# Kernel tuning notes

Hardware: AMD Instinct MI355X
Metric: run time of the kernel (lower is better)

Reference implementation:

```python
import jax, jax.numpy as jnp
import numpy as np
import math

D_MODEL = 512
N_HEADS = 8
D_FF = 2048
EPS = 1e-5

def _layernorm(x, g, b):
    m = jnp.mean(x, axis=-1, keepdims=True)
    v = jnp.var(x, axis=-1, keepdims=True)
    return (x - m) * jax.lax.rsqrt(v + EPS) * g + b

def setup_inputs() -> dict:
    key = jax.random.key(0)
    ks = jax.random.split(key, 8)
    d, dff = D_MODEL, D_FF
    s = lambda fan: 1.0 / math.sqrt(fan)
    return {
        "x": jax.random.normal(ks[0], (4, 2048, d), dtype=jnp.float32),
        "w_qkv": jax.random.normal(ks[1], (d, 3 * d), dtype=jnp.float32) * s(d),
        "b_qkv": jnp.zeros((3 * d,), dtype=jnp.float32),
        "w1": jax.random.normal(ks[2], (d, dff), dtype=jnp.float32) * s(d),
        "b1": jnp.zeros((dff,), dtype=jnp.float32),
        "w2": jax.random.normal(ks[3], (dff, d), dtype=jnp.float32) * s(dff),
        "b2": jnp.zeros((d,), dtype=jnp.float32),
        "g1": jnp.ones((d,), dtype=jnp.float32),
        "be1": jnp.zeros((d,), dtype=jnp.float32),
        "g2": jnp.ones((d,), dtype=jnp.float32),
        "be2": jnp.zeros((d,), dtype=jnp.float32),
    }

def reference(x, w_qkv, b_qkv, w1, b1, w2, b2, g1, be1, g2, be2):
    B, L, d = x.shape
    H = N_HEADS
    hd = d // H
    # Faithful to original: scale = 1/sqrt(hd), scores = qk / scale = qk * sqrt(hd)
    inv_scale = math.sqrt(hd)
    qkv = x @ w_qkv + b_qkv            # [B, L, 3d]
    q, k, v = jnp.split(qkv, 3, axis=-1)
    split_heads = lambda t: t.reshape(B, L, H, hd).transpose(0, 2, 1, 3)  # [B,H,L,hd]
    q, k, v = map(split_heads, (q, k, v))
    scores = jnp.einsum('bhqd,bhkd->bhqk', q, k) * inv_scale
    attn = jax.nn.softmax(scores, axis=-1)
    out = jnp.einsum('bhqk,bhkd->bhqd', attn, v)
    out = out.transpose(0, 2, 1, 3).reshape(B, L, d)
    x = _layernorm(x + out, g1, be1)
    ff = jax.nn.relu(x @ w1 + b1) @ w2 + b2
    return _layernorm(x + ff, g2, be2)
```

## Files before the change

### kernel.cpp

```cpp
#include <hip/hip_runtime.h>

typedef _Float16 f16;
typedef _Float16 f16x4 __attribute__((ext_vector_type(4)));
typedef _Float16 f16x8 __attribute__((ext_vector_type(8)));
typedef float    f32x4 __attribute__((ext_vector_type(4)));
typedef float    f32x16 __attribute__((ext_vector_type(16)));
typedef unsigned int u32x4 __attribute__((ext_vector_type(4)));

#define QK_SCALE 11.5416528f

__device__ __forceinline__ void g2l16(const void* g, void* l) {
  __builtin_amdgcn_global_load_lds(
      (__attribute__((address_space(1))) const unsigned int*)g,
      (__attribute__((address_space(3))) unsigned int*)l, 16, 0, 0);
}

__device__ __forceinline__ f32x4 mfma16(f16x8 a, f16x8 b, f32x4 c) {
  return __builtin_amdgcn_mfma_f32_16x16x32_f16(a, b, c, 0, 0, 0);
}
__device__ __forceinline__ f32x16 mfma32(f16x8 a, f16x8 b, f32x16 c) {
  return __builtin_amdgcn_mfma_f32_32x32x16_f16(a, b, c, 0, 0, 0);
}
__device__ __forceinline__ unsigned pkrtz(float a, float b) {
  auto t = __builtin_amdgcn_cvt_pkrtz(a, b);
  return *(unsigned*)&t;
}
__device__ __forceinline__ void swap32(unsigned& a, unsigned& b) {
  asm volatile("v_permlane32_swap_b32 %0, %1" : "+v"(a), "+v"(b));
}

__device__ __forceinline__ int swz64(int row, int c) { return row * 64 + ((c ^ (row & 7)) << 3); }
__device__ __forceinline__ int swz32(int row, int c) { return row * 32 + ((c ^ ((row >> 1) & 3)) << 3); }

__global__ __launch_bounds__(256) void k_split(const float* __restrict__ in,
                                               f16* __restrict__ hi, f16* __restrict__ lo, int n4) {
  int i = blockIdx.x * 256 + threadIdx.x;
  if (i >= n4) return;
  f32x4 v = ((const f32x4*)in)[i];
  f16x4 h, l;
#pragma unroll
  for (int j = 0; j < 4; ++j) {
    f16 hv = (f16)v[j];
    h[j] = hv;
    l[j] = (f16)(v[j] - (float)hv);
  }
  ((f16x4*)hi)[i] = h;
  ((f16x4*)lo)[i] = l;
}

template <bool WLO>
__global__ __launch_bounds__(256) void k_transpose_split(const float* __restrict__ in, int K, int N,
                                                         f16* __restrict__ oh, f16* __restrict__ ol) {
  __shared__ float t[32][33];
  const int tx = threadIdx.x, ty = threadIdx.y;
  const int n0 = blockIdx.x * 32, k0 = blockIdx.y * 32;
#pragma unroll
  for (int j = 0; j < 4; ++j)
    t[ty + j * 8][tx] = in[(size_t)(k0 + ty + j * 8) * N + n0 + tx];
  __syncthreads();
#pragma unroll
  for (int j = 0; j < 4; ++j) {
    float v = t[tx][ty + j * 8];
    f16 hv = (f16)v;
    size_t o = (size_t)(n0 + ty + j * 8) * K + k0 + tx;
    oh[o] = hv;
    if (WLO) ol[o] = (f16)(v - (float)hv);
  }
}

template <int EPI, bool SPLIT>
__global__ __launch_bounds__(256, SPLIT ? 2 : 3) void k_gemm(
    const f16* __restrict__ Ah, const f16* __restrict__ Al,
    const f16* __restrict__ Bh, const f16* __restrict__ Bl,
    const float* __restrict__ bias,
    float* __restrict__ outF, f16* __restrict__ outH,
    f16* __restrict__ oqh, f16* __restrict__ oql,
    f16* __restrict__ okh, f16* __restrict__ ovT,
    int M, int N, int K) {
  constexpr int NB = SPLIT ? 2 : 1;
  __shared__ f16 As[NB][128 * 32];
  __shared__ f16 Bs[NB][128 * 32];

  const int tid = threadIdx.x;
  const int bm = blockIdx.x, bn = blockIdx.y;
  const int w = tid >> 6, lane = tid & 63;
  const int wr = w >> 1, wc = w & 1;
  const int lrow = lane & 15, lgrp = lane >> 4;

  const bool useLo = SPLIT && !(EPI == 0 && bn >= 4);

  f32x4 acc[4][4] = {};

  const int nkt = K >> 5;
  for (int kt = 0; kt < nkt; ++kt) {
    __syncthreads();
    const int kk = kt << 5;
#pragma unroll
    for (int c = 0; c < 2; ++c) {
      const int i = tid + (c << 8);
      const int row = i >> 2;
      const int gch = ((i & 3) ^ ((i >> 3) & 3)) << 3;
      const size_t aoff = (size_t)(bm * 128 + row) * K + kk + gch;
      const size_t boff = (size_t)(bn * 128 + row) * K + kk + gch;
      g2l16(Ah + aoff, &As[0][i * 8]);
      g2l16(Bh + boff, &Bs[0][i * 8]);
      if (SPLIT)
        if (useLo) {
          g2l16(Al + aoff, &As[1][i * 8]);
          g2l16(Bl + boff, &Bs[1][i * 8]);
        }
    }
    __syncthreads();

    f16x8 a0[4], a1[4], b0[4], b1[4];
#pragma unroll
    for (int mf = 0; mf < 4; ++mf) {
      const int off = swz32(wr * 64 + mf * 16 + lrow, lgrp);
      a0[mf] = *(const f16x8*)&As[0][off];
      if (SPLIT)
        if (useLo) a1[mf] = *(const f16x8*)&As[SPLIT ? 1 : 0][off];
    }
#pragma unroll
    for (int nf = 0; nf < 4; ++nf) {
      const int off = swz32(wc * 64 + nf * 16 + lrow, lgrp);
      b0[nf] = *(const f16x8*)&Bs[0][off];
      if (SPLIT)
        if (useLo) b1[nf] = *(const f16x8*)&Bs[SPLIT ? 1 : 0][off];
    }
#pragma unroll
    for (int mf = 0; mf < 4; ++mf)
#pragma unroll
      for (int nf = 0; nf < 4; ++nf) {
        acc[mf][nf] = mfma16(a0[mf], b0[nf], acc[mf][nf]);
        if (SPLIT)
          if (useLo) {
            acc[mf][nf] = mfma16(a0[mf], b1[nf], acc[mf][nf]);
            acc[mf][nf] = mfma16(a1[mf], b0[nf], acc[mf][nf]);
          }
      }
  }

  const int rowbase = bm * 128 + wr * 64 + lgrp * 4;
  const int colbase = bn * 128 + wc * 64 + lrow;
#pragma unroll
  for (int mf = 0; mf < 4; ++mf) {
#pragma unroll
    for (int nf = 0; nf < 4; ++nf) {
      const int gc = colbase + nf * 16;
      const float bv = bias[gc];
#pragma unroll
      for (int r = 0; r < 4; ++r) {
        const int gr = rowbase + mf * 16 + r;
        const float val = acc[mf][nf][r] + bv;
        if (EPI == 0) {
          const int bb = gr >> 11, tok = gr & 2047;
          const int kind = gc >> 9, hh = (gc >> 6) & 7, dd = gc & 63;
          const size_t bhp = (size_t)((bb << 3) + hh);
          const size_t qidx = (bhp * 2048 + tok) * 64 + dd;
          if (kind == 0) {
            const float sv = val * QK_SCALE;
            const f16 hv = (f16)sv;
            oqh[qidx] = hv; oql[qidx] = (f16)(sv - (float)hv);
          } else if (kind == 1) {
            okh[qidx] = (f16)val;
          } else {
            ovT[(bhp * 64 + dd) * 2048 + tok] = (f16)val;
          }
        } else if (EPI == 1) {
          outH[(size_t)gr * N + gc] = (f16)fmaxf(val, 0.f);
        } else {
          outF[(size_t)gr * N + gc] = val;
        }
      }
    }
  }
}

__global__ __launch_bounds__(256, 2) void k_attn(
    const f16* __restrict__ Qh, const f16* __restrict__ Ql,
    const f16* __restrict__ Kh, const f16* __restrict__ Vt,
    float* __restrict__ out) {
  __shared__ f16 sK[4][64 * 64], sV[4][64 * 64];

  const int tid = threadIdx.x;
  const int wg = (blockIdx.x & 7) * 64 + (blockIdx.x >> 3);
  const int bh = wg >> 4, qt = wg & 15;
  const int w = tid >> 6, lane = tid & 63;
  const int lh = lane & 31, hh = lane >> 5;

  const int qrow = qt * 128 + w * 32 + lh;
  const size_t qoff = ((size_t)bh * 2048 + qrow) * 64;
  f16x8 qh8[4], ql8[4];
#pragma unroll
  for (int d = 0; d < 4; ++d) {
    const size_t o = qoff + d * 16 + hh * 8;
    qh8[d] = *(const f16x8*)(Qh + o);
    ql8[d] = *(const f16x8*)(Ql + o);
  }

  auto stage = [&](int b, int kt) {
    const size_t koff = ((size_t)bh * 2048 + (size_t)kt * 64) * 64;
    const size_t voff = (size_t)bh * 64 * 2048 + (size_t)kt * 64;
#pragma unroll
    for (int c = 0; c < 2; ++c) {
      const int i = tid + (c << 8);
      const int row = i >> 3;
      const int gch = ((i & 7) ^ (row & 7)) << 3;
      g2l16(Kh + koff + (size_t)row * 64 + gch, &sK[b][i * 8]);
      g2l16(Vt + voff + (size_t)row * 2048 + gch, &sV[b][i * 8]);
    }
  };

  stage(0, 0);
  stage(1, 1);
  stage(2, 2);

  float m_run = -3e38f;
  float l_run = 0.f;
  f32x16 oacc[2] = {};
  f32x16 sA[2] = {}, sB[2] = {};

  auto qk = [&](f32x16 (&s)[2], int bi) {
    __builtin_amdgcn_s_setprio(1);
#pragma unroll
    for (int d = 0; d < 4; ++d) {
      const f16x8 k0 = *(const f16x8*)&sK[bi][swz64(lh, d * 2 + hh)];
      const f16x8 k1 = *(const f16x8*)&sK[bi][swz64(32 + lh, d * 2 + hh)];
      s[0] = mfma32(k0, qh8[d], s[0]);
      s[0] = mfma32(k0, ql8[d], s[0]);
      s[1] = mfma32(k1, qh8[d], s[1]);
      s[1] = mfma32(k1, ql8[d], s[1]);
    }
    __builtin_amdgcn_s_setprio(0);
  };

  auto sm_pv = [&](f32x16 (&s)[2], int bi) {
    float mt = s[0][0];
#pragma unroll
    for (int r = 0; r < 16; ++r) { mt = fmaxf(mt, s[0][r]); mt = fmaxf(mt, s[1][r]); }
    mt = fmaxf(mt, __shfl_xor(mt, 32, 64));
    float mcur = m_run;
    if (!__all(mt <= mcur + 8.0f)) {
      const float mnew = fmaxf(mcur, mt);
      const float corr = __builtin_amdgcn_exp2f(mcur - mnew);
      m_run = mnew;
      l_run *= corr;
      oacc[0] = oacc[0] * corr;
      oacc[1] = oacc[1] * corr;
      mcur = mnew;
    }
    float ps = 0.f;
    unsigned pk0[8], pk1[8];
#pragma unroll
    for (int i = 0; i < 8; ++i) {
      const float a0 = __builtin_amdgcn_exp2f(s[0][2 * i] - mcur);
      const float a1 = __builtin_amdgcn_exp2f(s[0][2 * i + 1] - mcur);
      const float b0 = __builtin_amdgcn_exp2f(s[1][2 * i] - mcur);
      const float b1 = __builtin_amdgcn_exp2f(s[1][2 * i + 1] - mcur);
      ps += (a0 + a1) + (b0 + b1);
      pk0[i] = pkrtz(a0, a1);
      pk1[i] = pkrtz(b0, b1);
    }
    ps += __shfl_xor(ps, 32, 64);
    l_run += ps;
    s[0] = (f32x16){};
    s[1] = (f32x16){};

    swap32(pk0[0], pk0[2]); swap32(pk0[1], pk0[3]);
    swap32(pk0[4], pk0[6]); swap32(pk0[5], pk0[7]);
    swap32(pk1[0], pk1[2]); swap32(pk1[1], pk1[3]);
    swap32(pk1[4], pk1[6]); swap32(pk1[5], pk1[7]);

    u32x4 pbu[4];
    pbu[0] = (u32x4){pk0[0], pk0[1], pk0[2], pk0[3]};
    pbu[1] = (u32x4){pk0[4], pk0[5], pk0[6], pk0[7]};
    pbu[2] = (u32x4){pk1[0], pk1[1], pk1[2], pk1[3]};
    pbu[3] = (u32x4){pk1[4], pk1[5], pk1[6], pk1[7]};

    __builtin_amdgcn_s_setprio(1);
#pragma unroll
    for (int s2 = 0; s2 < 4; ++s2) {
      const f16x8 pb = *(const f16x8*)&pbu[s2];
#pragma unroll
      for (int db = 0; db < 2; ++db) {
        const f16x8 v = *(const f16x8*)&sV[bi][swz64(db * 32 + lh, s2 * 2 + hh)];
        oacc[db] = mfma32(v, pb, oacc[db]);
      }
    }
    __builtin_amdgcn_s_setprio(0);
  };

  auto endwait = [&](int t) {
    if (t < 29) {
      asm volatile("s_waitcnt vmcnt(4)" ::: "memory");
    } else {
      asm volatile("s_waitcnt vmcnt(0)" ::: "memory");
    }
    __builtin_amdgcn_sched_barrier(0);
    __builtin_amdgcn_s_barrier();
    __builtin_amdgcn_sched_barrier(0);
  };

  asm volatile("s_waitcnt vmcnt(4)" ::: "memory");
  __builtin_amdgcn_sched_barrier(0);
  __builtin_amdgcn_s_barrier();
  __builtin_amdgcn_sched_barrier(0);
  qk(sA, 0);

  for (int t = 0; t < 32; t += 2) {
    {
      if (t + 1 < 32) qk(sB, (t + 1) & 3);
      if (t + 3 < 32) stage((t + 3) & 3, t + 3);
      sm_pv(sA, t & 3);
      if (t + 1 < 32) endwait(t);
    }
    if (t + 1 < 32) {
      if (t + 2 < 32) qk(sA, (t + 2) & 3);
      if (t + 4 < 32) stage((t + 4) & 3, t + 4);
      sm_pv(sB, (t + 1) & 3);
      if (t + 2 < 32) endwait(t + 1);
    }
  }

  const int b = bh >> 3, hd = bh & 7;
  const float inv = 1.0f / l_run;
  const int trow = b * 2048 + qt * 128 + w * 32 + lh;
  float* po = out + (size_t)trow * 512 + hd * 64;
#pragma unroll
  for (int db = 0; db < 2; ++db)
#pragma unroll
    for (int rq = 0; rq < 4; ++rq) {
      f32x4 o;
#pragma unroll
      for (int j = 0; j < 4; ++j) o[j] = oacc[db][rq * 4 + j] * inv;
      *(f32x4*)(po + db * 32 + rq * 8 + hh * 4) = o;
    }
}

__global__ __launch_bounds__(64) void k_ln(const float* __restrict__ X, const float* __restrict__ R,
                                           const float* __restrict__ g, const float* __restrict__ be,
                                           float* __restrict__ outF, f16* __restrict__ outH) {
  const int row = blockIdx.x, t = threadIdx.x;
  const size_t base = (size_t)row * 512 + t * 8;
  f32x4 x0 = *(const f32x4*)(X + base);
  f32x4 x1 = *(const f32x4*)(X + base + 4);
  f32x4 r0 = *(const f32x4*)(R + base);
  f32x4 r1 = *(const f32x4*)(R + base + 4);
  x0 = x0 + r0;
  x1 = x1 + r1;
  float s = 0.f, ss = 0.f;
#pragma unroll
  for (int j = 0; j < 4; ++j) { s += x0[j] + x1[j]; ss += x0[j] * x0[j] + x1[j] * x1[j]; }
#pragma unroll
  for (int o = 32; o; o >>= 1) {
    s += __shfl_xor(s, o, 64);
    ss += __shfl_xor(ss, o, 64);
  }
  const float mean = s * (1.f / 512.f);
  const float var = ss * (1.f / 512.f) - mean * mean;
  const float rs = rsqrtf(var + 1e-5f);
  f32x4 g0 = *(const f32x4*)(g + t * 8);
  f32x4 g1v = *(const f32x4*)(g + t * 8 + 4);
  f32x4 b0 = *(const f32x4*)(be + t * 8);
  f32x4 b1 = *(const f32x4*)(be + t * 8 + 4);
  f32x4 y0 = (x0 - mean) * rs * g0 + b0;
  f32x4 y1 = (x1 - mean) * rs * g1v + b1;
  *(f32x4*)(outF + base) = y0;
  *(f32x4*)(outF + base + 4) = y1;
  if (outH != nullptr) {
    f16x8 hx;
#pragma unroll
    for (int j = 0; j < 4; ++j) { hx[j] = (f16)y0[j]; hx[j + 4] = (f16)y1[j]; }
    *(f16x8*)(outH + base) = hx;
  }
}

extern "C" void kernel_launch(void* const* d_in, const int* in_sizes, int n_in,
                              void* d_out, int out_size, void* d_ws, size_t ws_size,
                              hipStream_t stream) {
  (void)in_sizes; (void)n_in; (void)out_size;
  const float* x = (const float*)d_in[0];
  const float* w_qkv = (const float*)d_in[1];
  const float* b_qkv = (const float*)d_in[2];
  const float* w1 = (const float*)d_in[3];
  const float* b1 = (const float*)d_in[4];
  const float* w2 = (const float*)d_in[5];
  const float* b2 = (const float*)d_in[6];
  const float* g1 = (const float*)d_in[7];
  const float* be1 = (const float*)d_in[8];
  const float* g2 = (const float*)d_in[9];
  const float* be2 = (const float*)d_in[10];
  float* out = (float*)d_out;

  char* p = (char*)d_ws;
  auto take = [&](size_t bytes) {
    char* r = p;
    p += (bytes + 255) & ~(size_t)255;
    return r;
  };
  f16* xh = (f16*)take(8192ull * 512 * 2);
  f16* xl = (f16*)take(8192ull * 512 * 2);
  f16* wqkvTh = (f16*)take(1536ull * 512 * 2);
  f16* wqkvTl = (f16*)take(1536ull * 512 * 2);
  f16* w1T = (f16*)take(2048ull * 512 * 2);
  f16* w2T = (f16*)take(512ull * 2048 * 2);
  f16* qh = (f16*)take(32ull * 2048 * 64 * 2);
  f16* ql = (f16*)take(32ull * 2048 * 64 * 2);
  f16* kh = (f16*)take(32ull * 2048 * 64 * 2);
  f16* vT = (f16*)take(32ull * 64 * 2048 * 2);
  float* attn = (float*)take(8192ull * 512 * 4);
  float* x1f = (float*)take(8192ull * 512 * 4);
  f16* x1h = (f16*)take(8192ull * 512 * 2);
  f16* hbuf = qh;
  float* ffb = attn;

  if ((size_t)(p - (char*)d_ws) > ws_size) return;

  dim3 tb(32, 8);
  k_split<<<4096, 256, 0, stream>>>(x, xh, xl, 8192 * 512 / 4);
  k_transpose_split<true><<<dim3(1536 / 32, 512 / 32), tb, 0, stream>>>(w_qkv, 512, 1536, wqkvTh, wqkvTl);
  k_transpose_split<false><<<dim3(2048 / 32, 512 / 32), tb, 0, stream>>>(w1, 512, 2048, w1T, nullptr);
  k_transpose_split<false><<<dim3(512 / 32, 2048 / 32), tb, 0, stream>>>(w2, 2048, 512, w2T, nullptr);

  k_gemm<0, true><<<dim3(64, 12), 256, 0, stream>>>(xh, xl, wqkvTh, wqkvTl, b_qkv,
                                                    nullptr, nullptr, qh, ql, kh, vT,
                                                    8192, 1536, 512);
  k_attn<<<512, 256, 0, stream>>>(qh, ql, kh, vT, attn);
  k_ln<<<8192, 64, 0, stream>>>(x, attn, g1, be1, x1f, x1h);
  k_gemm<1, false><<<dim3(64, 16), 256, 0, stream>>>(x1h, nullptr, w1T, nullptr, b1,
                                                     nullptr, hbuf, nullptr, nullptr, nullptr, nullptr,
                                                     8192, 2048, 512);
  k_gemm<2, false><<<dim3(64, 4), 256, 0, stream>>>(hbuf, nullptr, w2T, nullptr, b2,
                                                    ffb, nullptr, nullptr, nullptr, nullptr, nullptr,
                                                    8192, 512, 2048);
  k_ln<<<8192, 64, 0, stream>>>(x1f, ffb, g2, be2, out, nullptr);
}
```

Before: 194.1 us.

## Split-K FFN2 GEMM, fp16 attention output, fused LN kernels, zero-init QK accumulators

```diff
diff --git a/kernel.cpp b/kernel.cpp
--- a/kernel.cpp
+++ b/kernel.cpp
@@ -73,16 +73,19 @@
     const f16* __restrict__ Ah, const f16* __restrict__ Al,
     const f16* __restrict__ Bh, const f16* __restrict__ Bl,
     const float* __restrict__ bias,
-    float* __restrict__ outF, f16* __restrict__ outH,
+    float* __restrict__ outF, float* __restrict__ outF2, f16* __restrict__ outH,
     f16* __restrict__ oqh, f16* __restrict__ oql,
     f16* __restrict__ okh, f16* __restrict__ ovT,
-    int M, int N, int K) {
+    int M, int N, int K, int ks) {
   constexpr int NB = SPLIT ? 2 : 1;
   __shared__ f16 As[NB][128 * 32];
   __shared__ f16 Bs[NB][128 * 32];
 
   const int tid = threadIdx.x;
   const int bm = blockIdx.x, bn = blockIdx.y;
+  const int bnc = (EPI == 3) ? (bn & 3) : bn;
+  const int half = (EPI == 3) ? (bn >> 2) : 0;
+  const int hoff = half * 1024;
   const int w = tid >> 6, lane = tid & 63;
   const int wr = w >> 1, wc = w & 1;
   const int lrow = lane & 15, lgrp = lane >> 4;
@@ -100,8 +103,8 @@
       const int i = tid + (c << 8);
       const int row = i >> 2;
       const int gch = ((i & 3) ^ ((i >> 3) & 3)) << 3;
-      const size_t aoff = (size_t)(bm * 128 + row) * K + kk + gch;
-      const size_t boff = (size_t)(bn * 128 + row) * K + kk + gch;
+      const size_t aoff = (size_t)(bm * 128 + row) * ks + hoff + kk + gch;
+      const size_t boff = (size_t)(bnc * 128 + row) * ks + hoff + kk + gch;
       g2l16(Ah + aoff, &As[0][i * 8]);
       g2l16(Bh + boff, &Bs[0][i * 8]);
       if (SPLIT)
@@ -141,13 +144,13 @@
   }
 
   const int rowbase = bm * 128 + wr * 64 + lgrp * 4;
-  const int colbase = bn * 128 + wc * 64 + lrow;
+  const int colbase = bnc * 128 + wc * 64 + lrow;
 #pragma unroll
   for (int mf = 0; mf < 4; ++mf) {
 #pragma unroll
     for (int nf = 0; nf < 4; ++nf) {
       const int gc = colbase + nf * 16;
-      const float bv = bias[gc];
+      const float bv = (EPI == 3 && half) ? 0.f : bias[gc];
 #pragma unroll
       for (int r = 0; r < 4; ++r) {
         const int gr = rowbase + mf * 16 + r;
@@ -168,8 +171,11 @@
           }
         } else if (EPI == 1) {
           outH[(size_t)gr * N + gc] = (f16)fmaxf(val, 0.f);
+        } else if (EPI == 2) {
+          outF[(size_t)gr * N + gc] = val;
         } else {
-          outF[(size_t)gr * N + gc] = val;
+          float* o = half ? outF2 : outF;
+          o[(size_t)gr * N + gc] = val;
         }
       }
     }
@@ -179,7 +185,7 @@
 __global__ __launch_bounds__(256, 2) void k_attn(
     const f16* __restrict__ Qh, const f16* __restrict__ Ql,
     const f16* __restrict__ Kh, const f16* __restrict__ Vt,
-    float* __restrict__ out) {
+    f16* __restrict__ out) {
   __shared__ f16 sK[4][64 * 64], sV[4][64 * 64];
 
   const int tid = threadIdx.x;
@@ -218,12 +224,21 @@
   float m_run = -3e38f;
   float l_run = 0.f;
   f32x16 oacc[2] = {};
+  const f32x16 kZero = {};
   f32x16 sA[2] = {}, sB[2] = {};
 
   auto qk = [&](f32x16 (&s)[2], int bi) {
     __builtin_amdgcn_s_setprio(1);
-#pragma unroll
-    for (int d = 0; d < 4; ++d) {
+    {
+      const f16x8 k0 = *(const f16x8*)&sK[bi][swz64(lh, hh)];
+      const f16x8 k1 = *(const f16x8*)&sK[bi][swz64(32 + lh, hh)];
+      s[0] = mfma32(k0, qh8[0], kZero);
+      s[0] = mfma32(k0, ql8[0], s[0]);
+      s[1] = mfma32(k1, qh8[0], kZero);
+      s[1] = mfma32(k1, ql8[0], s[1]);
+    }
+#pragma unroll
+    for (int d = 1; d < 4; ++d) {
       const f16x8 k0 = *(const f16x8*)&sK[bi][swz64(lh, d * 2 + hh)];
       const f16x8 k1 = *(const f16x8*)&sK[bi][swz64(32 + lh, d * 2 + hh)];
       s[0] = mfma32(k0, qh8[d], s[0]);
@@ -263,8 +278,6 @@
     }
     ps += __shfl_xor(ps, 32, 64);
     l_run += ps;
-    s[0] = (f32x16){};
-    s[1] = (f32x16){};
 
     swap32(pk0[0], pk0[2]); swap32(pk0[1], pk0[3]);
     swap32(pk0[4], pk0[6]); swap32(pk0[5], pk0[7]);
@@ -325,29 +338,71 @@
   const int b = bh >> 3, hd = bh & 7;
   const float inv = 1.0f / l_run;
   const int trow = b * 2048 + qt * 128 + w * 32 + lh;
-  float* po = out + (size_t)trow * 512 + hd * 64;
+  f16* po = out + (size_t)trow * 512 + hd * 64;
 #pragma unroll
   for (int db = 0; db < 2; ++db)
 #pragma unroll
     for (int rq = 0; rq < 4; ++rq) {
-      f32x4 o;
-#pragma unroll
-      for (int j = 0; j < 4; ++j) o[j] = oacc[db][rq * 4 + j] * inv;
-      *(f32x4*)(po + db * 32 + rq * 8 + hh * 4) = o;
-    }
-}
-
-__global__ __launch_bounds__(64) void k_ln(const float* __restrict__ X, const float* __restrict__ R,
-                                           const float* __restrict__ g, const float* __restrict__ be,
-                                           float* __restrict__ outF, f16* __restrict__ outH) {
-  const int row = blockIdx.x, t = threadIdx.x;
+      f16x4 o;
+#pragma unroll
+      for (int j = 0; j < 4; ++j) o[j] = (f16)(oacc[db][rq * 4 + j] * inv);
+      *(f16x4*)(po + db * 32 + rq * 8 + hh * 4) = o;
+    }
+}
+
+__global__ __launch_bounds__(256) void k_ln1(const float* __restrict__ X, const f16* __restrict__ R,
+                                             const float* __restrict__ g, const float* __restrict__ be,
+                                             f16* __restrict__ outH) {
+  const int row = blockIdx.x * 4 + (threadIdx.x >> 6);
+  const int t = threadIdx.x & 63;
   const size_t base = (size_t)row * 512 + t * 8;
   f32x4 x0 = *(const f32x4*)(X + base);
   f32x4 x1 = *(const f32x4*)(X + base + 4);
-  f32x4 r0 = *(const f32x4*)(R + base);
-  f32x4 r1 = *(const f32x4*)(R + base + 4);
-  x0 = x0 + r0;
-  x1 = x1 + r1;
+  const f16x8 r = *(const f16x8*)(R + base);
+#pragma unroll
+  for (int j = 0; j < 4; ++j) { x0[j] += (float)r[j]; x1[j] += (float)r[j + 4]; }
+  float s = 0.f, ss = 0.f;
+#pragma unroll
+  for (int j = 0; j < 4; ++j) { s += x0[j] + x1[j]; ss += x0[j] * x0[j] + x1[j] * x1[j]; }
+#pragma unroll
+  for (int o = 32; o; o >>= 1) {
+    s += __shfl_xor(s, o, 64);
+    ss += __shfl_xor(ss, o, 64);
+  }
+  const float mean = s * (1.f / 512.f);
+  const float var = ss * (1.f / 512.f) - mean * mean;
+  const float rs = rsqrtf(var + 1e-5f);
+  f32x4 g0 = *(const f32x4*)(g + t * 8);
+  f32x4 g1v = *(const f32x4*)(g + t * 8 + 4);
+  f32x4 b0 = *(const f32x4*)(be + t * 8);
+  f32x4 b1 = *(const f32x4*)(be + t * 8 + 4);
+  f16x8 hx;
+#pragma unroll
+  for (int j = 0; j < 4; ++j) {
+    hx[j] = (f16)((x0[j] - mean) * rs * g0[j] + b0[j]);
+    hx[j + 4] = (f16)((x1[j] - mean) * rs * g1v[j] + b1[j]);
+  }
+  *(f16x8*)(outH + base) = hx;
+}
+
+__global__ __launch_bounds__(256) void k_ln2(const f16* __restrict__ Xh,
+                                             const float* __restrict__ R0, const float* __restrict__ R1,
+                                             const float* __restrict__ g, const float* __restrict__ be,
+                                             float* __restrict__ out) {
+  const int row = blockIdx.x * 4 + (threadIdx.x >> 6);
+  const int t = threadIdx.x & 63;
+  const size_t base = (size_t)row * 512 + t * 8;
+  const f16x8 xv = *(const f16x8*)(Xh + base);
+  f32x4 r00 = *(const f32x4*)(R0 + base);
+  f32x4 r01 = *(const f32x4*)(R0 + base + 4);
+  f32x4 r10 = *(const f32x4*)(R1 + base);
+  f32x4 r11 = *(const f32x4*)(R1 + base + 4);
+  f32x4 x0, x1;
+#pragma unroll
+  for (int j = 0; j < 4; ++j) {
+    x0[j] = (float)xv[j] + r00[j] + r10[j];
+    x1[j] = (float)xv[j + 4] + r01[j] + r11[j];
+  }
   float s = 0.f, ss = 0.f;
 #pragma unroll
   for (int j = 0; j < 4; ++j) { s += x0[j] + x1[j]; ss += x0[j] * x0[j] + x1[j] * x1[j]; }
@@ -365,14 +420,8 @@
   f32x4 b1 = *(const f32x4*)(be + t * 8 + 4);
   f32x4 y0 = (x0 - mean) * rs * g0 + b0;
   f32x4 y1 = (x1 - mean) * rs * g1v + b1;
-  *(f32x4*)(outF + base) = y0;
-  *(f32x4*)(outF + base + 4) = y1;
-  if (outH != nullptr) {
-    f16x8 hx;
-#pragma unroll
-    for (int j = 0; j < 4; ++j) { hx[j] = (f16)y0[j]; hx[j + 4] = (f16)y1[j]; }
-    *(f16x8*)(outH + base) = hx;
-  }
+  *(f32x4*)(out + base) = y0;
+  *(f32x4*)(out + base + 4) = y1;
 }
 
 extern "C" void kernel_launch(void* const* d_in, const int* in_sizes, int n_in,
@@ -408,11 +457,11 @@
   f16* ql = (f16*)take(32ull * 2048 * 64 * 2);
   f16* kh = (f16*)take(32ull * 2048 * 64 * 2);
   f16* vT = (f16*)take(32ull * 64 * 2048 * 2);
-  float* attn = (float*)take(8192ull * 512 * 4);
-  float* x1f = (float*)take(8192ull * 512 * 4);
+  f16* attnH = (f16*)take(8192ull * 512 * 2);
   f16* x1h = (f16*)take(8192ull * 512 * 2);
+  float* ffb0 = (float*)take(8192ull * 512 * 4);
+  float* ffb1 = (float*)take(8192ull * 512 * 4);
   f16* hbuf = qh;
-  float* ffb = attn;
 
   if ((size_t)(p - (char*)d_ws) > ws_size) return;
 
@@ -423,15 +472,15 @@
   k_transpose_split<false><<<dim3(512 / 32, 2048 / 32), tb, 0, stream>>>(w2, 2048, 512, w2T, nullptr);
 
   k_gemm<0, true><<<dim3(64, 12), 256, 0, stream>>>(xh, xl, wqkvTh, wqkvTl, b_qkv,
-                                                    nullptr, nullptr, qh, ql, kh, vT,
-                                                    8192, 1536, 512);
-  k_attn<<<512, 256, 0, stream>>>(qh, ql, kh, vT, attn);
-  k_ln<<<8192, 64, 0, stream>>>(x, attn, g1, be1, x1f, x1h);
+                                                    nullptr, nullptr, nullptr, qh, ql, kh, vT,
+                                                    8192, 1536, 512, 512);
+  k_attn<<<512, 256, 0, stream>>>(qh, ql, kh, vT, attnH);
+  k_ln1<<<2048, 256, 0, stream>>>(x, attnH, g1, be1, x1h);
   k_gemm<1, false><<<dim3(64, 16), 256, 0, stream>>>(x1h, nullptr, w1T, nullptr, b1,
-                                                     nullptr, hbuf, nullptr, nullptr, nullptr, nullptr,
-                                                     8192, 2048, 512);
-  k_gemm<2, false><<<dim3(64, 4), 256, 0, stream>>>(hbuf, nullptr, w2T, nullptr, b2,
-                                                    ffb, nullptr, nullptr, nullptr, nullptr, nullptr,
-                                                    8192, 512, 2048);
-  k_ln<<<8192, 64, 0, stream>>>(x1f, ffb, g2, be2, out, nullptr);
-}
+                                                     nullptr, nullptr, hbuf, nullptr, nullptr, nullptr, nullptr,
+                                                     8192, 2048, 512, 512);
+  k_gemm<3, false><<<dim3(64, 8), 256, 0, stream>>>(hbuf, nullptr, w2T, nullptr, b2,
+                                                    ffb0, ffb1, nullptr, nullptr, nullptr, nullptr, nullptr,
+                                                    8192, 512, 1024, 2048);
+  k_ln2<<<2048, 256, 0, stream>>>(x1h, ffb0, ffb1, g2, be2, out);
+}
```

Result: faster. 179.2 us (-7.7%).
